# Kernel optimization log

Hardware: AMD Instinct MI355X
Metric: run time of the kernel (lower is better)

## Reference

```python
import jax, jax.numpy as jnp
import numpy as np

N_HEADS = 8
EPS = 1e-5


def setup_inputs() -> dict:
    key = jax.random.key(0)
    ks = jax.random.split(key, 5)
    c = 512
    x = jax.random.normal(ks[0], (2, c, 2, 32, 32), dtype=jnp.float32)
    s = 0.02
    Wq = jax.random.normal(ks[1], (c, c), dtype=jnp.float32) * s
    Wk = jax.random.normal(ks[2], (c, c), dtype=jnp.float32) * s
    Wv = jax.random.normal(ks[3], (c, c), dtype=jnp.float32) * s
    Wo = jax.random.normal(ks[4], (c, c), dtype=jnp.float32) * s
    bo = jnp.zeros((c,), dtype=jnp.float32)
    gamma = jnp.ones((c,), dtype=jnp.float32)
    beta = jnp.zeros((c,), dtype=jnp.float32)
    return {"x": x, "Wq": Wq, "Wk": Wk, "Wv": Wv, "Wo": Wo, "bo": bo,
            "gamma": gamma, "beta": beta}


def reference(x, Wq, Wk, Wv, Wo, bo, gamma, beta):
    b, c, d, h, w = x.shape
    seq = d * h * w
    # [b, c, d, h, w] -> [b, seq, c]
    xs = jnp.transpose(x, (0, 2, 3, 4, 1)).reshape(b, seq, c)
    # LayerNorm over channel dim
    mu = jnp.mean(xs, axis=-1, keepdims=True)
    var = jnp.mean(jnp.square(xs - mu), axis=-1, keepdims=True)
    xn = (xs - mu) * jax.lax.rsqrt(var + EPS) * gamma + beta
    # Self-attention (cond falls back to x); weights stored [in, out]
    dh = c // N_HEADS
    q = (xn @ Wq).reshape(b, seq, N_HEADS, dh)
    k = (xn @ Wk).reshape(b, seq, N_HEADS, dh)
    v = (xn @ Wv).reshape(b, seq, N_HEADS, dh)
    scale = dh ** (-0.5)
    attn = jnp.einsum('bihd,bjhd->bhij', q, k) * scale  # [b, H, seq, seq]
    attn = jax.nn.softmax(attn, axis=-1)
    out = jnp.einsum('bhij,bjhd->bihd', attn, v).reshape(b, seq, c)
    out = out @ Wo + bo
    y = out + xs  # residual
    return jnp.transpose(y.reshape(b, d, h, w, c), (0, 4, 1, 2, 3))
```

## Files before the change

kernel.cpp:

```cpp
#include <hip/hip_runtime.h>
#include <cstdint>

typedef unsigned short u16;
typedef __bf16 bf16x8 __attribute__((ext_vector_type(8)));
typedef float f32x4 __attribute__((ext_vector_type(4)));
typedef u16 u16x4 __attribute__((ext_vector_type(4)));
typedef u16 u16x8 __attribute__((ext_vector_type(8)));

__device__ __forceinline__ u16 f2bf(float f) {
  union { float f; unsigned u; } v; v.f = f;
  unsigned r = v.u + 0x7FFFu + ((v.u >> 16) & 1u);
  return (u16)(r >> 16);
}

__device__ __forceinline__ float bf2f(u16 u) {
  union { unsigned u; float f; } c; c.u = ((unsigned)u) << 16;
  return c.f;
}

__device__ __forceinline__ unsigned cvtpk(float lo, float hi) {
  unsigned r;
  asm("v_cvt_pk_bf16_f32 %0, %1, %2" : "=v"(r) : "v"(lo), "v"(hi));
  return r;
}

__device__ __forceinline__ f32x4 mfma16(bf16x8 a, bf16x8 b, f32x4 c) {
  return __builtin_amdgcn_mfma_f32_16x16x32_bf16(a, b, c, 0, 0, 0);
}

__device__ __forceinline__ void gload_lds16(const void* g, void* l) {
  auto* lp = reinterpret_cast<__attribute__((address_space(3))) unsigned int*>(
      reinterpret_cast<uintptr_t>(l));
  const auto* gp = reinterpret_cast<const __attribute__((address_space(1))) unsigned int*>(
      reinterpret_cast<uintptr_t>(g));
  __builtin_amdgcn_global_load_lds(gp, lp, 16, 0, 0);
}

template <int N>
__device__ __forceinline__ void waitcnt_vm() {
  if constexpr (N == 0)      asm volatile("s_waitcnt vmcnt(0)" ::: "memory");
  else if constexpr (N == 2) asm volatile("s_waitcnt vmcnt(2)" ::: "memory");
  else if constexpr (N == 4) asm volatile("s_waitcnt vmcnt(4)" ::: "memory");
  else if constexpr (N == 6) asm volatile("s_waitcnt vmcnt(6)" ::: "memory");
  else                       asm volatile("s_waitcnt vmcnt(8)" ::: "memory");
}

__global__ __launch_bounds__(256) void prep_kernel(const float* __restrict__ Wq,
                                                   const float* __restrict__ Wk,
                                                   const float* __restrict__ Wv,
                                                   const float* __restrict__ Wo,
                                                   const float* __restrict__ x,
                                                   const float* __restrict__ gamma,
                                                   const float* __restrict__ beta,
                                                   u16* __restrict__ wt_out,
                                                   u16* __restrict__ xn) {
  struct LnSh {
    float red0[16][16];
    float red1[16][16];
    float mu[16], rs[16];
    u16 tile[16][520];
  };
  struct WtSh { float tile[32][33]; };
  __shared__ __align__(16) char shraw[sizeof(LnSh) > sizeof(WtSh) ? sizeof(LnSh) : sizeof(WtSh)];
  int bid = blockIdx.x;
  int t = threadIdx.x;
  if (bid < 256) {
    LnSh& S = *reinterpret_cast<LnSh*>(shraw);
    int b = bid >> 7;
    int s0 = (bid & 127) * 16;
    int tx = t & 15, ty = t >> 4;
    const float* xb = x + (size_t)b * 512 * 2048 + s0 + tx;
    float vals[32];
    float sum = 0.f, sq = 0.f;
#pragma unroll
    for (int k = 0; k < 32; k++) {
      float v = xb[(size_t)(ty + k * 16) * 2048];
      vals[k] = v;
      sum += v; sq += v * v;
    }
    S.red0[ty][tx] = sum; S.red1[ty][tx] = sq;
    __syncthreads();
    if (t < 16) {
      float a = 0.f, c2 = 0.f;
#pragma unroll
      for (int i = 0; i < 16; i++) { a += S.red0[i][t]; c2 += S.red1[i][t]; }
      float mu = a * (1.f / 512.f);
      float var = c2 * (1.f / 512.f) - mu * mu;
      S.mu[t] = mu;
      S.rs[t] = rsqrtf(var + 1e-5f);
    }
    __syncthreads();
    float mu = S.mu[tx], rs = S.rs[tx];
#pragma unroll
    for (int k = 0; k < 32; k++) {
      int ch = ty + k * 16;
      S.tile[tx][ch] = f2bf((vals[k] - mu) * rs * gamma[ch] + beta[ch]);
    }
    __syncthreads();
    int col = (t & 63) * 8;
    int r0 = t >> 6;
    u16* outb = xn + (size_t)(b * 2048 + s0) * 512;
#pragma unroll
    for (int i = 0; i < 4; i++) {
      int row = r0 + 4 * i;
      *(u16x8*)(outb + (size_t)row * 512 + col) = *(const u16x8*)(&S.tile[row][col]);
    }
  } else {
    WtSh& S = *reinterpret_cast<WtSh*>(shraw);
    int wid = bid - 256;
    int z = wid >> 8;
    const float* W = (z == 0) ? Wq : (z == 1) ? Wk : (z == 2) ? Wv : Wo;
    u16* o = wt_out + (size_t)z * 262144;
    int rem = wid & 255;
    int n0 = (rem >> 4) * 32, k0 = (rem & 15) * 32;
    int tx = t & 31, ty = t >> 5;
#pragma unroll
    for (int i = 0; i < 4; i++)
      S.tile[ty + i * 8][tx] = W[(size_t)(k0 + ty + i * 8) * 512 + n0 + tx];
    __syncthreads();
#pragma unroll
    for (int i = 0; i < 4; i++) {
      int n = ty + i * 8;
      o[(size_t)(n0 + n) * 512 + k0 + tx] = f2bf(S.tile[tx][n]);
    }
  }
}

template <int AM, int AN>
__device__ __forceinline__ void gemm_tile_ring(const u16* __restrict__ A, const u16* __restrict__ B,
                                               int m0, int n0, f32x4 acc[AM][AN],
                                               u16* As, u16* Bs) {
  constexpr int BM = AM * 32, BN = AN * 32;
  constexpr int LA = BM / 64, LB = BN / 64;
  constexpr int L = LA + LB;
  int t = threadIdx.x;
  int w = t >> 6, lane = t & 63;
  int wm = w >> 1, wn = w & 1;
  int arow = t >> 2;
  int acol = (t & 3) * 8;
  int lrow = lane & 15;
  int lko = (lane >> 4) * 8;

  auto stage = [&](int buf, int k0) {
#pragma unroll
    for (int g = 0; g < LA; ++g)
      gload_lds16(A + (size_t)(m0 + g * 64 + arow) * 512 + k0 + acol,
                  As + buf * (BM * 32) + g * 2048 + w * 512);
#pragma unroll
    for (int g = 0; g < LB; ++g)
      gload_lds16(B + (size_t)(n0 + g * 64 + arow) * 512 + k0 + acol,
                  Bs + buf * (BN * 32) + g * 2048 + w * 512);
  };

  stage(0, 0);
  stage(1, 32);
  stage(2, 64);
  __syncthreads();

  for (int tt = 0; tt < 16; ++tt) {
    int pk = (tt + 3 < 16) ? (tt + 3) * 32 : 0;
    stage((tt + 3) & 3, pk);
    const u16* as = As + (tt & 3) * (BM * 32);
    const u16* bs = Bs + (tt & 3) * (BN * 32);
    bf16x8 af[AM], bfr[AN];
#pragma unroll
    for (int i = 0; i < AM; i++) af[i] = *(const bf16x8*)(as + (wm * (AM * 16) + i * 16 + lrow) * 32 + lko);
#pragma unroll
    for (int j = 0; j < AN; j++) bfr[j] = *(const bf16x8*)(bs + (wn * (AN * 16) + j * 16 + lrow) * 32 + lko);
    __builtin_amdgcn_s_setprio(1);
#pragma unroll
    for (int i = 0; i < AM; i++)
#pragma unroll
      for (int j = 0; j < AN; j++)
        acc[i][j] = mfma16(af[i], bfr[j], acc[i][j]);
    __builtin_amdgcn_s_setprio(0);
    waitcnt_vm<2 * L>();
    __builtin_amdgcn_s_barrier();
  }
  waitcnt_vm<0>();
}

__global__ __launch_bounds__(256) void gemm_qkv(const u16* __restrict__ xn, const u16* __restrict__ wt,
                                                u16* __restrict__ Qb, u16* __restrict__ Kp,
                                                u16* __restrict__ Vp) {
  __shared__ u16 As[4 * 64 * 32];
  __shared__ u16 Bs[4 * 128 * 32];
  const float SCQ = 0.125f * 1.4426950408889634f;
  int mat = blockIdx.z;
  const u16* WT = wt + (size_t)mat * 262144;
  int m0 = blockIdx.x * 64, n0 = blockIdx.y * 128;
  f32x4 acc[2][4] = {};
  gemm_tile_ring<2, 4>(xn, WT, m0, n0, acc, As, Bs);
  int t = threadIdx.x, w = t >> 6, lane = t & 63;
  int wm = w >> 1, wn = w & 1, lrow = lane & 15, lgrp = lane >> 4;
#pragma unroll
  for (int i = 0; i < 2; i++) {
#pragma unroll
    for (int j = 0; j < 4; j++) {
      int gr0 = m0 + wm * 32 + i * 16 + lgrp * 4;
      int gc = n0 + wn * 64 + j * 16 + lrow;
      if (mat == 0) {
#pragma unroll
        for (int r = 0; r < 4; r++)
          Qb[(size_t)(gr0 + r) * 512 + gc] = f2bf(acc[i][j][r] * SCQ);
      } else if (mat == 1) {
        int h = gc >> 6, d = gc & 63;
        int half = d >> 5, lg = (d >> 3) & 3, jj = d & 7;
#pragma unroll
        for (int r = 0; r < 4; r++) {
          int kg = gr0 + r;
          int bq = kg >> 11, kl = kg & 2047;
          int kt = kl >> 5, kw = kl & 31;
          int tt = (kw >> 2) & 1;
          int kwb = kw - 4 * tt;
          int lr = ((kwb >> 3) << 2) | (kwb & 3);
          int c = 2 * tt + half;
          size_t idx = ((size_t)((bq * 8 + h) * 64 + kt) * 4 + c) * 512 + (lg * 16 + lr) * 8 + jj;
          Kp[idx] = f2bf(acc[i][j][r]);
        }
      } else {
        int h = gc >> 6, d = gc & 63;
        int dt = d >> 4, lr = d & 15;
        int kg = gr0;
        int bq = kg >> 11, kl = kg & 2047;
        int kt = kl >> 5, kw = kl & 31;
        int lg = kw >> 3, j0 = kw & 7;
        u16x4 v;
#pragma unroll
        for (int r = 0; r < 4; r++) v[r] = f2bf(acc[i][j][r]);
        size_t idx = ((size_t)((bq * 8 + h) * 64 + kt) * 4 + dt) * 512 + (lg * 16 + lr) * 8 + j0;
        *(u16x4*)(Vp + idx) = v;
      }
    }
  }
}

__global__ __launch_bounds__(256, 3) void attn_kernel(const u16* __restrict__ Qb, const u16* __restrict__ Kp,
                                                      const u16* __restrict__ Vp, u16* __restrict__ Opart,
                                                      float* __restrict__ ml, int logS) {
  int S = 1 << logS;
  int bid = blockIdx.x;
  int qt = bid >> (4 + logS);
  int group = bid & (16 * S - 1);
  int hb = group >> logS, sp = group & (S - 1);
  int b = hb >> 3, h = hb & 7;
  int kt0 = sp * (64 >> logS);
  int nsteps = 64 >> logS;

  int t = threadIdx.x, w = t >> 6, lane = t & 63;
  int lrow = lane & 15, lgrp = lane >> 4, lko = lgrp * 8;
  int q0 = qt * 128 + w * 32;

  const u16* Qp = Qb + (size_t)(b * 2048 + q0 + lrow) * 512 + h * 64 + lko;
  bf16x8 qa0 = *(const bf16x8*)(Qp);
  bf16x8 qa1 = *(const bf16x8*)(Qp + 32);
  bf16x8 qb0 = *(const bf16x8*)(Qp + 16 * 512);
  bf16x8 qb1 = *(const bf16x8*)(Qp + 16 * 512 + 32);

  const u16* Kbh = Kp + (size_t)hb * 131072 + lane * 8;
  const u16* Vbh = Vp + (size_t)hb * 131072 + lane * 8;

  f32x4 acca[4] = {}, accb[4] = {};
  float lsum_a = 0.f, lsum_b = 0.f;

  bf16x8 kA[4], vA[4], kB[4], vB[4];

  auto loadKV = [&](bf16x8* kf, bf16x8* vf, int st) {
    const u16* pk = Kbh + (size_t)(kt0 + st) * 2048;
    const u16* pv = Vbh + (size_t)(kt0 + st) * 2048;
#pragma unroll
    for (int c = 0; c < 4; c++) kf[c] = *(const bf16x8*)(pk + c * 512);
#pragma unroll
    for (int c = 0; c < 4; c++) vf[c] = *(const bf16x8*)(pv + c * 512);
  };

  auto computeStep = [&](const bf16x8* kc, const bf16x8* vc) {
    f32x4 sa0 = {}, sa1 = {}, sb0 = {}, sb1 = {};
    __builtin_amdgcn_s_setprio(1);
    sa0 = mfma16(kc[0], qa0, sa0);
    sa0 = mfma16(kc[1], qa1, sa0);
    sa1 = mfma16(kc[2], qa0, sa1);
    sa1 = mfma16(kc[3], qa1, sa1);
    sb0 = mfma16(kc[0], qb0, sb0);
    sb0 = mfma16(kc[1], qb1, sb0);
    sb1 = mfma16(kc[2], qb0, sb1);
    sb1 = mfma16(kc[3], qb1, sb1);
    __builtin_amdgcn_s_setprio(0);

    float pa[8], pb8[8];
#pragma unroll
    for (int jj = 0; jj < 4; jj++) pa[jj] = exp2f(sa0[jj]);
#pragma unroll
    for (int jj = 0; jj < 4; jj++) pa[4 + jj] = exp2f(sa1[jj]);
#pragma unroll
    for (int jj = 0; jj < 4; jj++) pb8[jj] = exp2f(sb0[jj]);
#pragma unroll
    for (int jj = 0; jj < 4; jj++) pb8[4 + jj] = exp2f(sb1[jj]);
    lsum_a += ((pa[0] + pa[1]) + (pa[2] + pa[3])) + ((pa[4] + pa[5]) + (pa[6] + pa[7]));
    lsum_b += ((pb8[0] + pb8[1]) + (pb8[2] + pb8[3])) + ((pb8[4] + pb8[5]) + (pb8[6] + pb8[7]));

    union { unsigned u[4]; bf16x8 v; } pua, pub;
    pua.u[0] = cvtpk(pa[0], pa[1]); pua.u[1] = cvtpk(pa[2], pa[3]);
    pua.u[2] = cvtpk(pa[4], pa[5]); pua.u[3] = cvtpk(pa[6], pa[7]);
    pub.u[0] = cvtpk(pb8[0], pb8[1]); pub.u[1] = cvtpk(pb8[2], pb8[3]);
    pub.u[2] = cvtpk(pb8[4], pb8[5]); pub.u[3] = cvtpk(pb8[6], pb8[7]);

    __builtin_amdgcn_s_setprio(1);
    acca[0] = mfma16(pua.v, vc[0], acca[0]);
    acca[1] = mfma16(pua.v, vc[1], acca[1]);
    acca[2] = mfma16(pua.v, vc[2], acca[2]);
    acca[3] = mfma16(pua.v, vc[3], acca[3]);
    accb[0] = mfma16(pub.v, vc[0], accb[0]);
    accb[1] = mfma16(pub.v, vc[1], accb[1]);
    accb[2] = mfma16(pub.v, vc[2], accb[2]);
    accb[3] = mfma16(pub.v, vc[3], accb[3]);
    __builtin_amdgcn_s_setprio(0);
  };

  loadKV(kA, vA, 0);
  for (int st = 0; st < nsteps; st += 2) {
    loadKV(kB, vB, (st + 1 < nsteps) ? st + 1 : 0);
    computeStep(kA, vA);
    loadKV(kA, vA, (st + 2 < nsteps) ? st + 2 : 0);
    computeStep(kB, vB);
  }

  lsum_a += __shfl_xor(lsum_a, 16); lsum_a += __shfl_xor(lsum_a, 32);
  lsum_b += __shfl_xor(lsum_b, 16); lsum_b += __shfl_xor(lsum_b, 32);

  if (lgrp == 0) {
    int row = b * 2048 + q0 + lrow;
    ml[(size_t)sp * 32768 + row * 8 + h] = lsum_a;
    ml[(size_t)sp * 32768 + (row + 16) * 8 + h] = lsum_b;
  }

  u16* Ao = Opart + (size_t)sp * 2097152 + (size_t)(b * 2048 + q0) * 512 + h * 64;
#pragma unroll
  for (int r = 0; r < 4; r++) {
#pragma unroll
    for (int dt = 0; dt < 4; dt++) {
      Ao[(size_t)(lgrp * 4 + r) * 512 + dt * 16 + lrow] = f2bf(acca[dt][r]);
      Ao[(size_t)(16 + lgrp * 4 + r) * 512 + dt * 16 + lrow] = f2bf(accb[dt][r]);
    }
  }
}

template <int S>
__global__ __launch_bounds__(256) void attn_combine(const u16* __restrict__ Opart,
                                                    const float* __restrict__ ml,
                                                    u16* __restrict__ AO) {
  int gid = blockIdx.x * 256 + threadIdx.x;
  int pair = gid >> 3, dcol = (gid & 7) * 8;
  int row = pair >> 3, h = pair & 7;
  float lsum = 0.f;
#pragma unroll
  for (int s = 0; s < S; s++) lsum += ml[(size_t)s * 32768 + pair];
  float inv = 1.0f / lsum;
  float o[8] = {};
#pragma unroll
  for (int s = 0; s < S; s++) {
    u16x8 ov = *(const u16x8*)(Opart + (size_t)s * 2097152 + (size_t)row * 512 + h * 64 + dcol);
#pragma unroll
    for (int j = 0; j < 8; j++) o[j] += bf2f(ov[j]);
  }
  u16x8 outv;
#pragma unroll
  for (int j = 0; j < 8; j++) outv[j] = f2bf(o[j] * inv);
  *(u16x8*)(AO + (size_t)row * 512 + h * 64 + dcol) = outv;
}

__global__ __launch_bounds__(256) void gemm_out(const u16* __restrict__ AO, const u16* __restrict__ WoT,
                                                const float* __restrict__ bo, const float* __restrict__ x,
                                                float* __restrict__ y) {
  __shared__ u16 As[4 * 64 * 32];
  __shared__ u16 Bs[4 * 64 * 32];
  int m0 = blockIdx.x * 64, n0 = blockIdx.y * 64;
  f32x4 acc[2][2] = {};
  gemm_tile_ring<2, 2>(AO, WoT, m0, n0, acc, As, Bs);
  int t = threadIdx.x, w = t >> 6, lane = t & 63;
  int wm = w >> 1, wn = w & 1, lrow = lane & 15, lgrp = lane >> 4;
#pragma unroll
  for (int i = 0; i < 2; i++) {
#pragma unroll
    for (int j = 0; j < 2; j++) {
      int gr0 = m0 + wm * 32 + i * 16 + lgrp * 4;
      int gc = n0 + wn * 32 + j * 16 + lrow;
      int bb = gr0 >> 11, s = gr0 & 2047;
      float bias = bo[gc];
      const float* xp = x + ((size_t)bb * 512 + gc) * 2048 + s;
      float4 xv = *(const float4*)xp;
      float4 o;
      o.x = acc[i][j][0] + bias + xv.x;
      o.y = acc[i][j][1] + bias + xv.y;
      o.z = acc[i][j][2] + bias + xv.z;
      o.w = acc[i][j][3] + bias + xv.w;
      *(float4*)(y + ((size_t)bb * 512 + gc) * 2048 + s) = o;
    }
  }
}

extern "C" void kernel_launch(void* const* d_in, const int* in_sizes, int n_in,
                              void* d_out, int out_size, void* d_ws, size_t ws_size,
                              hipStream_t stream) {
  const float* x = (const float*)d_in[0];
  const float* Wq = (const float*)d_in[1];
  const float* Wk = (const float*)d_in[2];
  const float* Wv = (const float*)d_in[3];
  const float* Wo = (const float*)d_in[4];
  const float* bo = (const float*)d_in[5];
  const float* gamma = (const float*)d_in[6];
  const float* beta = (const float*)d_in[7];
  float* y = (float*)d_out;
  char* ws = (char*)d_ws;
  u16* xn = (u16*)(ws);
  u16* wt = (u16*)(ws + (4 << 20));
  u16* Qb = (u16*)(ws + (6 << 20));
  u16* Kp = (u16*)(ws + (10 << 20));
  u16* Vp = (u16*)(ws + (14 << 20));
  u16* AO = (u16*)(ws + (18 << 20));
  float* ml = (float*)(ws + (22 << 20));
  u16* Opart = (u16*)(ws + (23 << 20));

  int logS;
  if (ws_size >= (40u << 20)) logS = 2;
  else if (ws_size >= (32u << 20)) logS = 1;
  else { logS = 0; Opart = AO; }

  prep_kernel<<<dim3(1280), dim3(256), 0, stream>>>(Wq, Wk, Wv, Wo, x, gamma, beta, wt, xn);
  gemm_qkv<<<dim3(64, 4, 3), dim3(256), 0, stream>>>(xn, wt, Qb, Kp, Vp);
  attn_kernel<<<dim3(256 << logS), dim3(256), 0, stream>>>(Qb, Kp, Vp, Opart, ml, logS);
  if (logS == 2)      attn_combine<4><<<dim3(1024), dim3(256), 0, stream>>>(Opart, ml, AO);
  else if (logS == 1) attn_combine<2><<<dim3(1024), dim3(256), 0, stream>>>(Opart, ml, AO);
  else                attn_combine<1><<<dim3(1024), dim3(256), 0, stream>>>(Opart, ml, AO);
  gemm_out<<<dim3(64, 8), dim3(256), 0, stream>>>(AO, wt + 3 * 262144, bo, x, y);
}
```

Baseline: 66.06 us.

## Double query rows per warp in attention to reuse K/V fragments

Each warp now handles 64 query rows (four 16-row subtiles) instead of 32, so every K/V fragment loaded from global memory feeds twice as many MFMAs. The grid is halved to match, and launch bounds drop from 3 to 2 blocks per SIMD to leave room for the larger accumulator and Q register footprint. The aim is to cut K/V load traffic per unit of compute. In exchange there are fewer blocks, lower occupancy and less latency hiding, with only 128<<logS blocks spread over the GPU.

```diff
diff --git a/kernel.cpp b/kernel.cpp
--- a/kernel.cpp
+++ b/kernel.cpp
@@ -235,7 +235,7 @@
   }
 }
 
-__global__ __launch_bounds__(256, 3) void attn_kernel(const u16* __restrict__ Qb, const u16* __restrict__ Kp,
+__global__ __launch_bounds__(256, 2) void attn_kernel(const u16* __restrict__ Qb, const u16* __restrict__ Kp,
                                                       const u16* __restrict__ Vp, u16* __restrict__ Opart,
                                                       float* __restrict__ ml, int logS) {
   int S = 1 << logS;
@@ -249,19 +249,21 @@
 
   int t = threadIdx.x, w = t >> 6, lane = t & 63;
   int lrow = lane & 15, lgrp = lane >> 4, lko = lgrp * 8;
-  int q0 = qt * 128 + w * 32;
+  int q0 = qt * 256 + w * 64;
 
   const u16* Qp = Qb + (size_t)(b * 2048 + q0 + lrow) * 512 + h * 64 + lko;
-  bf16x8 qa0 = *(const bf16x8*)(Qp);
-  bf16x8 qa1 = *(const bf16x8*)(Qp + 32);
-  bf16x8 qb0 = *(const bf16x8*)(Qp + 16 * 512);
-  bf16x8 qb1 = *(const bf16x8*)(Qp + 16 * 512 + 32);
+  bf16x8 qf[4][2];
+#pragma unroll
+  for (int s4 = 0; s4 < 4; s4++) {
+    qf[s4][0] = *(const bf16x8*)(Qp + (size_t)s4 * 16 * 512);
+    qf[s4][1] = *(const bf16x8*)(Qp + (size_t)s4 * 16 * 512 + 32);
+  }
 
   const u16* Kbh = Kp + (size_t)hb * 131072 + lane * 8;
   const u16* Vbh = Vp + (size_t)hb * 131072 + lane * 8;
 
-  f32x4 acca[4] = {}, accb[4] = {};
-  float lsum_a = 0.f, lsum_b = 0.f;
+  f32x4 acc[4][4] = {};
+  float lsum[4] = {0.f, 0.f, 0.f, 0.f};
 
   bf16x8 kA[4], vA[4], kB[4], vB[4];
 
@@ -275,46 +277,34 @@
   };
 
   auto computeStep = [&](const bf16x8* kc, const bf16x8* vc) {
-    f32x4 sa0 = {}, sa1 = {}, sb0 = {}, sb1 = {};
-    __builtin_amdgcn_s_setprio(1);
-    sa0 = mfma16(kc[0], qa0, sa0);
-    sa0 = mfma16(kc[1], qa1, sa0);
-    sa1 = mfma16(kc[2], qa0, sa1);
-    sa1 = mfma16(kc[3], qa1, sa1);
-    sb0 = mfma16(kc[0], qb0, sb0);
-    sb0 = mfma16(kc[1], qb1, sb0);
-    sb1 = mfma16(kc[2], qb0, sb1);
-    sb1 = mfma16(kc[3], qb1, sb1);
-    __builtin_amdgcn_s_setprio(0);
-
-    float pa[8], pb8[8];
-#pragma unroll
-    for (int jj = 0; jj < 4; jj++) pa[jj] = exp2f(sa0[jj]);
-#pragma unroll
-    for (int jj = 0; jj < 4; jj++) pa[4 + jj] = exp2f(sa1[jj]);
-#pragma unroll
-    for (int jj = 0; jj < 4; jj++) pb8[jj] = exp2f(sb0[jj]);
-#pragma unroll
-    for (int jj = 0; jj < 4; jj++) pb8[4 + jj] = exp2f(sb1[jj]);
-    lsum_a += ((pa[0] + pa[1]) + (pa[2] + pa[3])) + ((pa[4] + pa[5]) + (pa[6] + pa[7]));
-    lsum_b += ((pb8[0] + pb8[1]) + (pb8[2] + pb8[3])) + ((pb8[4] + pb8[5]) + (pb8[6] + pb8[7]));
-
-    union { unsigned u[4]; bf16x8 v; } pua, pub;
-    pua.u[0] = cvtpk(pa[0], pa[1]); pua.u[1] = cvtpk(pa[2], pa[3]);
-    pua.u[2] = cvtpk(pa[4], pa[5]); pua.u[3] = cvtpk(pa[6], pa[7]);
-    pub.u[0] = cvtpk(pb8[0], pb8[1]); pub.u[1] = cvtpk(pb8[2], pb8[3]);
-    pub.u[2] = cvtpk(pb8[4], pb8[5]); pub.u[3] = cvtpk(pb8[6], pb8[7]);
-
-    __builtin_amdgcn_s_setprio(1);
-    acca[0] = mfma16(pua.v, vc[0], acca[0]);
-    acca[1] = mfma16(pua.v, vc[1], acca[1]);
-    acca[2] = mfma16(pua.v, vc[2], acca[2]);
-    acca[3] = mfma16(pua.v, vc[3], acca[3]);
-    accb[0] = mfma16(pub.v, vc[0], accb[0]);
-    accb[1] = mfma16(pub.v, vc[1], accb[1]);
-    accb[2] = mfma16(pub.v, vc[2], accb[2]);
-    accb[3] = mfma16(pub.v, vc[3], accb[3]);
-    __builtin_amdgcn_s_setprio(0);
+#pragma unroll
+    for (int s4 = 0; s4 < 4; s4++) {
+      f32x4 s0 = {}, s1 = {};
+      __builtin_amdgcn_s_setprio(1);
+      s0 = mfma16(kc[0], qf[s4][0], s0);
+      s0 = mfma16(kc[1], qf[s4][1], s0);
+      s1 = mfma16(kc[2], qf[s4][0], s1);
+      s1 = mfma16(kc[3], qf[s4][1], s1);
+      __builtin_amdgcn_s_setprio(0);
+
+      float p[8];
+#pragma unroll
+      for (int jj = 0; jj < 4; jj++) p[jj] = exp2f(s0[jj]);
+#pragma unroll
+      for (int jj = 0; jj < 4; jj++) p[4 + jj] = exp2f(s1[jj]);
+      lsum[s4] += ((p[0] + p[1]) + (p[2] + p[3])) + ((p[4] + p[5]) + (p[6] + p[7]));
+
+      union { unsigned u[4]; bf16x8 v; } pu;
+      pu.u[0] = cvtpk(p[0], p[1]); pu.u[1] = cvtpk(p[2], p[3]);
+      pu.u[2] = cvtpk(p[4], p[5]); pu.u[3] = cvtpk(p[6], p[7]);
+
+      __builtin_amdgcn_s_setprio(1);
+      acc[s4][0] = mfma16(pu.v, vc[0], acc[s4][0]);
+      acc[s4][1] = mfma16(pu.v, vc[1], acc[s4][1]);
+      acc[s4][2] = mfma16(pu.v, vc[2], acc[s4][2]);
+      acc[s4][3] = mfma16(pu.v, vc[3], acc[s4][3]);
+      __builtin_amdgcn_s_setprio(0);
+    }
   };
 
   loadKV(kA, vA, 0);
@@ -325,22 +315,27 @@
     computeStep(kB, vB);
   }
 
-  lsum_a += __shfl_xor(lsum_a, 16); lsum_a += __shfl_xor(lsum_a, 32);
-  lsum_b += __shfl_xor(lsum_b, 16); lsum_b += __shfl_xor(lsum_b, 32);
+#pragma unroll
+  for (int s4 = 0; s4 < 4; s4++) {
+    lsum[s4] += __shfl_xor(lsum[s4], 16);
+    lsum[s4] += __shfl_xor(lsum[s4], 32);
+  }
 
   if (lgrp == 0) {
     int row = b * 2048 + q0 + lrow;
-    ml[(size_t)sp * 32768 + row * 8 + h] = lsum_a;
-    ml[(size_t)sp * 32768 + (row + 16) * 8 + h] = lsum_b;
+#pragma unroll
+    for (int s4 = 0; s4 < 4; s4++)
+      ml[(size_t)sp * 32768 + (row + s4 * 16) * 8 + h] = lsum[s4];
   }
 
   u16* Ao = Opart + (size_t)sp * 2097152 + (size_t)(b * 2048 + q0) * 512 + h * 64;
 #pragma unroll
-  for (int r = 0; r < 4; r++) {
-#pragma unroll
-    for (int dt = 0; dt < 4; dt++) {
-      Ao[(size_t)(lgrp * 4 + r) * 512 + dt * 16 + lrow] = f2bf(acca[dt][r]);
-      Ao[(size_t)(16 + lgrp * 4 + r) * 512 + dt * 16 + lrow] = f2bf(accb[dt][r]);
+  for (int s4 = 0; s4 < 4; s4++) {
+#pragma unroll
+    for (int r = 0; r < 4; r++) {
+#pragma unroll
+      for (int dt = 0; dt < 4; dt++)
+        Ao[(size_t)(s4 * 16 + lgrp * 4 + r) * 512 + dt * 16 + lrow] = f2bf(acc[s4][dt][r]);
     }
   }
 }
@@ -428,7 +423,7 @@
 
   prep_kernel<<<dim3(1280), dim3(256), 0, stream>>>(Wq, Wk, Wv, Wo, x, gamma, beta, wt, xn);
   gemm_qkv<<<dim3(64, 4, 3), dim3(256), 0, stream>>>(xn, wt, Qb, Kp, Vp);
-  attn_kernel<<<dim3(256 << logS), dim3(256), 0, stream>>>(Qb, Kp, Vp, Opart, ml, logS);
+  attn_kernel<<<dim3(128 << logS), dim3(256), 0, stream>>>(Qb, Kp, Vp, Opart, ml, logS);
   if (logS == 2)      attn_combine<4><<<dim3(1024), dim3(256), 0, stream>>>(Opart, ml, AO);
   else if (logS == 1) attn_combine<2><<<dim3(1024), dim3(256), 0, stream>>>(Opart, ml, AO);
   else                attn_combine<1><<<dim3(1024), dim3(256), 0, stream>>>(Opart, ml, AO);
```

Result: no change. 67.21 us (+1.7%).

## Store Q/K/V in fp8 and run attention MFMAs in fp8

Applied to the files above, without the earlier changes.

The QKV projection now writes Q, K and V as fp8 (e4m3) instead of bf16, keeping the same element-indexed packed layouts. The attention kernel loads 8-byte fp8 fragments and uses the fp8 16x16x32 MFMA for both QK^T and PV. The softmax probabilities are also packed to fp8. Occupancy is raised from 3 to 4 blocks per SM through launch bounds. The aim is to halve K/V/Q memory traffic and use the higher fp8 matrix throughput, at the cost of a notable precision loss in scores and probabilities that may exceed tolerance.

```diff
diff --git a/kernel.cpp b/kernel.cpp
--- a/kernel.cpp
+++ b/kernel.cpp
@@ -2,6 +2,7 @@
 #include <cstdint>
 
 typedef unsigned short u16;
+typedef unsigned char u8;
 typedef __bf16 bf16x8 __attribute__((ext_vector_type(8)));
 typedef float f32x4 __attribute__((ext_vector_type(4)));
 typedef u16 u16x4 __attribute__((ext_vector_type(4)));
@@ -18,14 +19,16 @@
   return c.f;
 }
 
-__device__ __forceinline__ unsigned cvtpk(float lo, float hi) {
-  unsigned r;
-  asm("v_cvt_pk_bf16_f32 %0, %1, %2" : "=v"(r) : "v"(lo), "v"(hi));
-  return r;
-}
-
 __device__ __forceinline__ f32x4 mfma16(bf16x8 a, bf16x8 b, f32x4 c) {
   return __builtin_amdgcn_mfma_f32_16x16x32_bf16(a, b, c, 0, 0, 0);
+}
+
+__device__ __forceinline__ f32x4 mfma8(long a, long b, f32x4 c) {
+  return __builtin_amdgcn_mfma_f32_16x16x32_fp8_fp8(a, b, c, 0, 0, 0);
+}
+
+__device__ __forceinline__ u8 f2fp8(float f) {
+  return (u8)(__builtin_amdgcn_cvt_pk_fp8_f32(f, f, 0, false) & 0xff);
 }
 
 __device__ __forceinline__ void gload_lds16(const void* g, void* l) {
@@ -181,8 +184,8 @@
 }
 
 __global__ __launch_bounds__(256) void gemm_qkv(const u16* __restrict__ xn, const u16* __restrict__ wt,
-                                                u16* __restrict__ Qb, u16* __restrict__ Kp,
-                                                u16* __restrict__ Vp) {
+                                                u8* __restrict__ Qb, u8* __restrict__ Kp,
+                                                u8* __restrict__ Vp) {
   __shared__ u16 As[4 * 64 * 32];
   __shared__ u16 Bs[4 * 128 * 32];
   const float SCQ = 0.125f * 1.4426950408889634f;
@@ -202,7 +205,7 @@
       if (mat == 0) {
 #pragma unroll
         for (int r = 0; r < 4; r++)
-          Qb[(size_t)(gr0 + r) * 512 + gc] = f2bf(acc[i][j][r] * SCQ);
+          Qb[(size_t)(gr0 + r) * 512 + gc] = f2fp8(acc[i][j][r] * SCQ);
       } else if (mat == 1) {
         int h = gc >> 6, d = gc & 63;
         int half = d >> 5, lg = (d >> 3) & 3, jj = d & 7;
@@ -216,7 +219,7 @@
           int lr = ((kwb >> 3) << 2) | (kwb & 3);
           int c = 2 * tt + half;
           size_t idx = ((size_t)((bq * 8 + h) * 64 + kt) * 4 + c) * 512 + (lg * 16 + lr) * 8 + jj;
-          Kp[idx] = f2bf(acc[i][j][r]);
+          Kp[idx] = f2fp8(acc[i][j][r]);
         }
       } else {
         int h = gc >> 6, d = gc & 63;
@@ -225,18 +228,17 @@
         int bq = kg >> 11, kl = kg & 2047;
         int kt = kl >> 5, kw = kl & 31;
         int lg = kw >> 3, j0 = kw & 7;
-        u16x4 v;
-#pragma unroll
-        for (int r = 0; r < 4; r++) v[r] = f2bf(acc[i][j][r]);
+        unsigned u = __builtin_amdgcn_cvt_pk_fp8_f32(acc[i][j][0], acc[i][j][1], 0, false);
+        u = __builtin_amdgcn_cvt_pk_fp8_f32(acc[i][j][2], acc[i][j][3], u, true);
         size_t idx = ((size_t)((bq * 8 + h) * 64 + kt) * 4 + dt) * 512 + (lg * 16 + lr) * 8 + j0;
-        *(u16x4*)(Vp + idx) = v;
+        *(unsigned*)(Vp + idx) = u;
       }
     }
   }
 }
 
-__global__ __launch_bounds__(256, 3) void attn_kernel(const u16* __restrict__ Qb, const u16* __restrict__ Kp,
-                                                      const u16* __restrict__ Vp, u16* __restrict__ Opart,
+__global__ __launch_bounds__(256, 4) void attn_kernel(const u8* __restrict__ Qb, const u8* __restrict__ Kp,
+                                                      const u8* __restrict__ Vp, u16* __restrict__ Opart,
                                                       float* __restrict__ ml, int logS) {
   int S = 1 << logS;
   int bid = blockIdx.x;
@@ -251,40 +253,40 @@
   int lrow = lane & 15, lgrp = lane >> 4, lko = lgrp * 8;
   int q0 = qt * 128 + w * 32;
 
-  const u16* Qp = Qb + (size_t)(b * 2048 + q0 + lrow) * 512 + h * 64 + lko;
-  bf16x8 qa0 = *(const bf16x8*)(Qp);
-  bf16x8 qa1 = *(const bf16x8*)(Qp + 32);
-  bf16x8 qb0 = *(const bf16x8*)(Qp + 16 * 512);
-  bf16x8 qb1 = *(const bf16x8*)(Qp + 16 * 512 + 32);
-
-  const u16* Kbh = Kp + (size_t)hb * 131072 + lane * 8;
-  const u16* Vbh = Vp + (size_t)hb * 131072 + lane * 8;
+  const u8* Qp = Qb + (size_t)(b * 2048 + q0 + lrow) * 512 + h * 64 + lko;
+  long qa0 = *(const long*)(Qp);
+  long qa1 = *(const long*)(Qp + 32);
+  long qb0 = *(const long*)(Qp + 16 * 512);
+  long qb1 = *(const long*)(Qp + 16 * 512 + 32);
+
+  const u8* Kbh = Kp + (size_t)hb * 131072 + lane * 8;
+  const u8* Vbh = Vp + (size_t)hb * 131072 + lane * 8;
 
   f32x4 acca[4] = {}, accb[4] = {};
   float lsum_a = 0.f, lsum_b = 0.f;
 
-  bf16x8 kA[4], vA[4], kB[4], vB[4];
-
-  auto loadKV = [&](bf16x8* kf, bf16x8* vf, int st) {
-    const u16* pk = Kbh + (size_t)(kt0 + st) * 2048;
-    const u16* pv = Vbh + (size_t)(kt0 + st) * 2048;
-#pragma unroll
-    for (int c = 0; c < 4; c++) kf[c] = *(const bf16x8*)(pk + c * 512);
-#pragma unroll
-    for (int c = 0; c < 4; c++) vf[c] = *(const bf16x8*)(pv + c * 512);
+  long kA[4], vA[4], kB[4], vB[4];
+
+  auto loadKV = [&](long* kf, long* vf, int st) {
+    const u8* pk = Kbh + (size_t)(kt0 + st) * 2048;
+    const u8* pv = Vbh + (size_t)(kt0 + st) * 2048;
+#pragma unroll
+    for (int c = 0; c < 4; c++) kf[c] = *(const long*)(pk + c * 512);
+#pragma unroll
+    for (int c = 0; c < 4; c++) vf[c] = *(const long*)(pv + c * 512);
   };
 
-  auto computeStep = [&](const bf16x8* kc, const bf16x8* vc) {
+  auto computeStep = [&](const long* kc, const long* vc) {
     f32x4 sa0 = {}, sa1 = {}, sb0 = {}, sb1 = {};
     __builtin_amdgcn_s_setprio(1);
-    sa0 = mfma16(kc[0], qa0, sa0);
-    sa0 = mfma16(kc[1], qa1, sa0);
-    sa1 = mfma16(kc[2], qa0, sa1);
-    sa1 = mfma16(kc[3], qa1, sa1);
-    sb0 = mfma16(kc[0], qb0, sb0);
-    sb0 = mfma16(kc[1], qb1, sb0);
-    sb1 = mfma16(kc[2], qb0, sb1);
-    sb1 = mfma16(kc[3], qb1, sb1);
+    sa0 = mfma8(kc[0], qa0, sa0);
+    sa0 = mfma8(kc[1], qa1, sa0);
+    sa1 = mfma8(kc[2], qa0, sa1);
+    sa1 = mfma8(kc[3], qa1, sa1);
+    sb0 = mfma8(kc[0], qb0, sb0);
+    sb0 = mfma8(kc[1], qb1, sb0);
+    sb1 = mfma8(kc[2], qb0, sb1);
+    sb1 = mfma8(kc[3], qb1, sb1);
     __builtin_amdgcn_s_setprio(0);
 
     float pa[8], pb8[8];
@@ -299,21 +301,26 @@
     lsum_a += ((pa[0] + pa[1]) + (pa[2] + pa[3])) + ((pa[4] + pa[5]) + (pa[6] + pa[7]));
     lsum_b += ((pb8[0] + pb8[1]) + (pb8[2] + pb8[3])) + ((pb8[4] + pb8[5]) + (pb8[6] + pb8[7]));
 
-    union { unsigned u[4]; bf16x8 v; } pua, pub;
-    pua.u[0] = cvtpk(pa[0], pa[1]); pua.u[1] = cvtpk(pa[2], pa[3]);
-    pua.u[2] = cvtpk(pa[4], pa[5]); pua.u[3] = cvtpk(pa[6], pa[7]);
-    pub.u[0] = cvtpk(pb8[0], pb8[1]); pub.u[1] = cvtpk(pb8[2], pb8[3]);
-    pub.u[2] = cvtpk(pb8[4], pb8[5]); pub.u[3] = cvtpk(pb8[6], pb8[7]);
+    unsigned alo = __builtin_amdgcn_cvt_pk_fp8_f32(pa[0], pa[1], 0, false);
+    alo = __builtin_amdgcn_cvt_pk_fp8_f32(pa[2], pa[3], alo, true);
+    unsigned ahi = __builtin_amdgcn_cvt_pk_fp8_f32(pa[4], pa[5], 0, false);
+    ahi = __builtin_amdgcn_cvt_pk_fp8_f32(pa[6], pa[7], ahi, true);
+    long pla = (long)(((unsigned long long)ahi << 32) | alo);
+    unsigned blo = __builtin_amdgcn_cvt_pk_fp8_f32(pb8[0], pb8[1], 0, false);
+    blo = __builtin_amdgcn_cvt_pk_fp8_f32(pb8[2], pb8[3], blo, true);
+    unsigned bhi = __builtin_amdgcn_cvt_pk_fp8_f32(pb8[4], pb8[5], 0, false);
+    bhi = __builtin_amdgcn_cvt_pk_fp8_f32(pb8[6], pb8[7], bhi, true);
+    long plb = (long)(((unsigned long long)bhi << 32) | blo);
 
     __builtin_amdgcn_s_setprio(1);
-    acca[0] = mfma16(pua.v, vc[0], acca[0]);
-    acca[1] = mfma16(pua.v, vc[1], acca[1]);
-    acca[2] = mfma16(pua.v, vc[2], acca[2]);
-    acca[3] = mfma16(pua.v, vc[3], acca[3]);
-    accb[0] = mfma16(pub.v, vc[0], accb[0]);
-    accb[1] = mfma16(pub.v, vc[1], accb[1]);
-    accb[2] = mfma16(pub.v, vc[2], accb[2]);
-    accb[3] = mfma16(pub.v, vc[3], accb[3]);
+    acca[0] = mfma8(pla, vc[0], acca[0]);
+    acca[1] = mfma8(pla, vc[1], acca[1]);
+    acca[2] = mfma8(pla, vc[2], acca[2]);
+    acca[3] = mfma8(pla, vc[3], acca[3]);
+    accb[0] = mfma8(plb, vc[0], accb[0]);
+    accb[1] = mfma8(plb, vc[1], accb[1]);
+    accb[2] = mfma8(plb, vc[2], accb[2]);
+    accb[3] = mfma8(plb, vc[3], accb[3]);
     __builtin_amdgcn_s_setprio(0);
   };
 
@@ -414,9 +421,9 @@
   char* ws = (char*)d_ws;
   u16* xn = (u16*)(ws);
   u16* wt = (u16*)(ws + (4 << 20));
-  u16* Qb = (u16*)(ws + (6 << 20));
-  u16* Kp = (u16*)(ws + (10 << 20));
-  u16* Vp = (u16*)(ws + (14 << 20));
+  u8* Qb = (u8*)(ws + (6 << 20));
+  u8* Kp = (u8*)(ws + (10 << 20));
+  u8* Vp = (u8*)(ws + (14 << 20));
   u16* AO = (u16*)(ws + (18 << 20));
   float* ml = (float*)(ws + (22 << 20));
   u16* Opart = (u16*)(ws + (23 << 20));
```

Result: no change. 65.15 us (-1.4%).
